# Optimization experiments

Measured on AMD Instinct MI355X. Metric: run time of the kernel, lower is better.

Reference implementation:

```python
import jax, jax.numpy as jnp
import numpy as np

N_NODES = 50000
N_EDGES = 800000
IN_DIM = 128
HEADS = 4
OUT_DIM = 32
NEG_SLOPE = 0.2


def setup_inputs() -> dict:
    key = jax.random.key(0)
    k_x, k_e, k_w, k_as, k_ad = jax.random.split(key, 5)
    x = jax.random.normal(k_x, (N_NODES, IN_DIM), dtype=jnp.float32)
    edge_index = jax.random.randint(k_e, (2, N_EDGES), 0, N_NODES, dtype=jnp.int32)
    # Linear(in_dim, heads*out_dim, bias=False): store as [in_dim, heads*out_dim]
    W = jax.random.normal(k_w, (IN_DIM, HEADS * OUT_DIM), dtype=jnp.float32) * 0.05
    a_src = jax.random.normal(k_as, (HEADS, OUT_DIM), dtype=jnp.float32) * 0.01
    a_dst = jax.random.normal(k_ad, (HEADS, OUT_DIM), dtype=jnp.float32) * 0.01
    return {"x": x, "edge_index": edge_index, "W": W, "a_src": a_src, "a_dst": a_dst}


def reference(x, edge_index, W, a_src, a_dst):
    N = x.shape[0]
    H, D = a_src.shape
    src, dst = edge_index[0], edge_index[1]
    h = (x @ W).reshape(N, H, D)                      # [N, H, D]
    h_src = h[src]                                    # [E, H, D] gather
    h_dst = h[dst]                                    # [E, H, D] gather
    e = jnp.einsum('ehd,hd->eh', h_src, a_src) + jnp.einsum('ehd,hd->eh', h_dst, a_dst)
    e = jax.nn.leaky_relu(e, NEG_SLOPE)               # [E, H]
    # segment softmax over dst, per head (vectorized across heads)
    m = jax.ops.segment_max(e, dst, num_segments=N)   # [N, H]
    exp = jnp.exp(e - m[dst])                         # [E, H]
    s = jax.ops.segment_sum(exp, dst, num_segments=N) # [N, H]
    alpha = exp / (s[dst] + 1e-12)                    # [E, H]
    # dropout p=0.0 -> identity
    out = jax.ops.segment_sum(alpha[:, :, None] * h_src, dst, num_segments=N)  # [N, H, D]
    return out.mean(axis=1)                           # [N, D]
```

## Files before the change

### kernel.cpp

```cpp
#include <hip/hip_runtime.h>
#include <hip/hip_bf16.h>

#define IN_DIM 128
#define HEADS 4
#define ODIM 32
#define HD (HEADS * ODIM)
#define NEG_SLOPE 0.2f

#define GM 64
#define LDK 136
#define ACCW 132

#define BIN_SHIFT 5
#define BIN_NODES 32
#define BINCAP 1024
#define MAXBINS 2048
#define KE 16

#define SMEM_BYTES 52224

typedef unsigned short ushortT;
typedef __attribute__((ext_vector_type(8))) short bf16x8;
typedef __attribute__((ext_vector_type(4))) float f32x4;

static __device__ __forceinline__ ushortT f2bf(float f) {
    __hip_bfloat16 b = __float2bfloat16(f);
    return *reinterpret_cast<ushortT*>(&b);
}
static __device__ __forceinline__ float hsel(float4 v, int head) {
    return (head == 0) ? v.x : (head == 1) ? v.y : (head == 2) ? v.z : v.w;
}
static __device__ __forceinline__ float i8f(unsigned int p, int sh) {
    return (float)((int)(p << (24 - sh)) >> 24);
}

__global__ void __launch_bounds__(256) k_wconv_zero(
    const float* __restrict__ W, ushortT* __restrict__ Wt_g,
    int* __restrict__ bin_cursor, int nbins)
{
    const int idx = blockIdx.x * 256 + threadIdx.x;
    const int c = idx >> 7, k = idx & 127;
    Wt_g[c * 128 + k] = f2bf(W[k * HD + c]);
    if (idx < nbins) bin_cursor[idx] = 0;
}

__global__ void __launch_bounds__(256) k_mega(
    const float* __restrict__ x, const ushortT* __restrict__ Wt_g,
    const float* __restrict__ a_src, const float* __restrict__ a_dst,
    const int* __restrict__ src, const int* __restrict__ dst,
    unsigned char* __restrict__ h8, float* __restrict__ scales,
    float* __restrict__ s_src, float* __restrict__ s_dst,
    int* __restrict__ bin_cursor, int* __restrict__ bin_buf,
    int N, int E, int nbins, int nBinBlocks)
{
    __shared__ __align__(16) char smem[SMEM_BYTES];
    const int t = threadIdx.x;

    if ((int)blockIdx.x < nBinBlocks) {
        int* lcnt = reinterpret_cast<int*>(smem);
        int* lcur = lcnt + MAXBINS;
        for (int i = t; i < nbins; i += 256) lcnt[i] = 0;
        __syncthreads();

        const int base_e = blockIdx.x * (256 * KE);
        int b_[KE]; int p_[KE];
#pragma unroll
        for (int k = 0; k < KE; ++k) {
            const int e = base_e + k * 256 + t;
            if (e < E) {
                const int d = dst[e];
                const int s = src[e];
                b_[k] = d >> BIN_SHIFT;
                p_[k] = ((d & (BIN_NODES - 1)) << 16) | s;
                atomicAdd(&lcnt[b_[k]], 1);
            } else {
                b_[k] = -1;
            }
        }
        __syncthreads();
        for (int i = t; i < nbins; i += 256) {
            const int c = lcnt[i];
            lcur[i] = (c > 0) ? atomicAdd(&bin_cursor[i], c) : 0;
        }
        __syncthreads();
#pragma unroll
        for (int k = 0; k < KE; ++k) {
            if (b_[k] >= 0) {
                const int pos = atomicAdd(&lcur[b_[k]], 1);
                if (pos < BINCAP) bin_buf[b_[k] * BINCAP + pos] = p_[k];
            }
        }
        return;
    }

    ushortT* Xs = reinterpret_cast<ushortT*>(smem);
    ushortT* Wt = Xs + GM * LDK;

    const int n0 = ((int)blockIdx.x - nBinBlocks) * GM;

    {
#pragma unroll
        for (int it = 0; it < 8; ++it) {
            const int o = it * 2048 + t * 8;
            *reinterpret_cast<uint4*>(&Wt[(o >> 7) * LDK + (o & 127)]) =
                *reinterpret_cast<const uint4*>(&Wt_g[o]);
        }
    }
    {
        const int r  = t >> 2;
        const int k0 = (t & 3) * 32;
        const int ng = n0 + r;
        if (ng < N) {
#pragma unroll
            for (int kk = 0; kk < 32; kk += 4) {
                float4 v = *reinterpret_cast<const float4*>(
                    &x[(size_t)ng * IN_DIM + k0 + kk]);
                ushort4 u;
                u.x = f2bf(v.x); u.y = f2bf(v.y); u.z = f2bf(v.z); u.w = f2bf(v.w);
                *reinterpret_cast<ushort4*>(&Xs[r * LDK + k0 + kk]) = u;
            }
        } else {
#pragma unroll
            for (int kk = 0; kk < 32; kk += 4)
                *reinterpret_cast<ushort4*>(&Xs[r * LDK + k0 + kk]) =
                    make_ushort4(0, 0, 0, 0);
        }
    }
    __syncthreads();

    const int w  = t >> 6;
    const int l  = t & 63;
    const int lr = l & 15;
    const int lk = (l >> 4) * 8;

    f32x4 acc[8];
#pragma unroll
    for (int i = 0; i < 8; ++i) acc[i] = (f32x4)(0.f);

#pragma unroll
    for (int kt = 0; kt < 4; ++kt) {
        const bf16x8 af = *reinterpret_cast<const bf16x8*>(
            &Xs[(w * 16 + lr) * LDK + kt * 32 + lk]);
#pragma unroll
        for (int ct = 0; ct < 8; ++ct) {
            const bf16x8 bfr = *reinterpret_cast<const bf16x8*>(
                &Wt[(ct * 16 + lr) * LDK + kt * 32 + lk]);
            acc[ct] = __builtin_amdgcn_mfma_f32_16x16x32_bf16(af, bfr, acc[ct],
                                                              0, 0, 0);
        }
    }

    float aSv[8], aDv[8];
#pragma unroll
    for (int ct = 0; ct < 8; ++ct) {
        aSv[ct] = a_src[ct * 16 + lr];
        aDv[ct] = a_dst[ct * 16 + lr];
    }
    const int rbase = w * 16 + (l >> 4) * 4;

#pragma unroll
    for (int j = 0; j < 4; ++j) {
        const int ng = n0 + rbase + j;
        float ps[4] = {0.f, 0.f, 0.f, 0.f}, pd[4] = {0.f, 0.f, 0.f, 0.f};
#pragma unroll
        for (int ct = 0; ct < 8; ++ct) {
            ps[ct >> 1] = fmaf(acc[ct][j], aSv[ct], ps[ct >> 1]);
            pd[ct >> 1] = fmaf(acc[ct][j], aDv[ct], pd[ct >> 1]);
        }
#pragma unroll
        for (int o = 1; o <= 8; o <<= 1) {
#pragma unroll
            for (int hh = 0; hh < 4; ++hh) {
                ps[hh] += __shfl_xor(ps[hh], o, 64);
                pd[hh] += __shfl_xor(pd[hh], o, 64);
            }
        }
        if (lr == 0 && ng < N) {
            *reinterpret_cast<float4*>(&s_src[ng * 4]) =
                make_float4(ps[0], ps[1], ps[2], ps[3]);
            *reinterpret_cast<float4*>(&s_dst[ng * 4]) =
                make_float4(pd[0], pd[1], pd[2], pd[3]);
        }
    }

    __syncthreads();
    float* accb = reinterpret_cast<float*>(smem);

#pragma unroll
    for (int ct = 0; ct < 8; ++ct)
#pragma unroll
        for (int j = 0; j < 4; ++j)
            accb[(rbase + j) * ACCW + ct * 16 + lr] = acc[ct][j];
    __syncthreads();

    {
        const int row = t >> 2;
        const int c0  = (t & 3) * 32;
        const int ng  = n0 + row;

        float4 v[8];
        float m = 0.f;
#pragma unroll
        for (int i = 0; i < 8; ++i) {
            v[i] = *reinterpret_cast<const float4*>(&accb[row * ACCW + c0 + 4 * i]);
            m = fmaxf(m, fmaxf(fmaxf(fabsf(v[i].x), fabsf(v[i].y)),
                               fmaxf(fabsf(v[i].z), fabsf(v[i].w))));
        }
        m = fmaxf(m, __shfl_xor(m, 1, 64));
        m = fmaxf(m, __shfl_xor(m, 2, 64));

        const float inv = (m > 0.f) ? 127.f / m : 0.f;
        unsigned int p[8];
#pragma unroll
        for (int i = 0; i < 8; ++i) {
            const int q0 = __float2int_rn(v[i].x * inv);
            const int q1 = __float2int_rn(v[i].y * inv);
            const int q2 = __float2int_rn(v[i].z * inv);
            const int q3 = __float2int_rn(v[i].w * inv);
            p[i] = (q0 & 0xFF) | ((q1 & 0xFF) << 8) |
                   ((q2 & 0xFF) << 16) | ((q3 & 0xFF) << 24);
        }
        if (ng < N) {
            *reinterpret_cast<uint4*>(&h8[(size_t)ng * 128 + c0]) =
                make_uint4(p[0], p[1], p[2], p[3]);
            *reinterpret_cast<uint4*>(&h8[(size_t)ng * 128 + c0 + 16]) =
                make_uint4(p[4], p[5], p[6], p[7]);
            if ((t & 3) == 0) scales[ng] = m * (1.f / 127.f);
        }
    }
}

__global__ void __launch_bounds__(256) k_pull_binned(
    const int* __restrict__ bin_buf, const int* __restrict__ bin_cursor,
    const unsigned char* __restrict__ h8, const float* __restrict__ scales,
    const float* __restrict__ s_src, const float* __restrict__ s_dst,
    float* __restrict__ out, int N)
{
    __shared__ ushortT csr[BINCAP];
    __shared__ int cnt_s[BIN_NODES], start_s[BIN_NODES], cur_s[BIN_NODES];

    const int b = blockIdx.x;
    const int t = threadIdx.x;
    const int node0 = b << BIN_SHIFT;

    int nedge = bin_cursor[b];
    nedge = (nedge < BINCAP) ? nedge : BINCAP;

    if (t < BIN_NODES) cnt_s[t] = 0;
    __syncthreads();

    for (int i = t; i < nedge; i += 256)
        atomicAdd(&cnt_s[bin_buf[b * BINCAP + i] >> 16], 1);
    __syncthreads();

    if (t < 32) {
        const int v = cnt_s[t];
        int inc = v;
#pragma unroll
        for (int o = 1; o < 32; o <<= 1) {
            const int x = __shfl_up(inc, o, 32);
            if (t >= o) inc += x;
        }
        start_s[t] = inc - v;
        cur_s[t]   = inc - v;
    }
    __syncthreads();

    for (int i = t; i < nedge; i += 256) {
        const int p = bin_buf[b * BINCAP + i];
        const int pos = atomicAdd(&cur_s[p >> 16], 1);
        csr[pos] = (ushortT)(p & 0xFFFF);
    }
    __syncthreads();

    const int wv   = t >> 6;
    const int l    = t & 63;
    const int half = l >> 5;
    const int l32  = l & 31;
    const int head = l32 >> 3;
    const int hoff = head * 8 + (l32 & 7);

    const unsigned int* hu = reinterpret_cast<const unsigned int*>(h8);
    const float4* ss4 = reinterpret_cast<const float4*>(s_src);

    for (int k = 0; k < 8; ++k) {
        const int nloc = wv * 8 + k;
        const int n = node0 + nloc;
        if (n >= N) break;

        const int st  = start_s[nloc];
        const int deg = cnt_s[nloc];
        const float4 vd4 = reinterpret_cast<const float4*>(s_dst)[n];
        const float vd = hsel(vd4, head);

        float den = 0.f;
        float a0 = 0.f, a1 = 0.f, a2 = 0.f, a3 = 0.f;

        const int count = (deg - half + 1) >> 1;
        for (int j = 0; j < count; j += 4) {
            const int i0 = st + 2 * j + half;
            const bool v1 = (j + 1) < count;
            const bool v2 = (j + 2) < count;
            const bool v3 = (j + 3) < count;
            const int s0 = csr[i0];
            const int s1 = v1 ? csr[i0 + 2] : s0;
            const int s2 = v2 ? csr[i0 + 4] : s0;
            const int s3 = v3 ? csr[i0 + 6] : s0;

            const float4 w0 = ss4[s0];
            const float4 w1 = ss4[s1];
            const float4 w2 = ss4[s2];
            const float4 w3 = ss4[s3];
            const float sc0 = scales[s0];
            const float sc1 = scales[s1];
            const float sc2 = scales[s2];
            const float sc3 = scales[s3];
            const unsigned int q0 = hu[(size_t)s0 * 32 + hoff];
            const unsigned int q1 = hu[(size_t)s1 * 32 + hoff];
            const unsigned int q2 = hu[(size_t)s2 * 32 + hoff];
            const unsigned int q3 = hu[(size_t)s3 * 32 + hoff];

            float e0 = hsel(w0, head) + vd;
            float e1 = hsel(w1, head) + vd;
            float e2 = hsel(w2, head) + vd;
            float e3 = hsel(w3, head) + vd;
            e0 = (e0 > 0.f) ? e0 : NEG_SLOPE * e0;
            e1 = (e1 > 0.f) ? e1 : NEG_SLOPE * e1;
            e2 = (e2 > 0.f) ? e2 : NEG_SLOPE * e2;
            e3 = (e3 > 0.f) ? e3 : NEG_SLOPE * e3;
            const float x0 = __expf(e0);
            const float x1 = v1 ? __expf(e1) : 0.f;
            const float x2 = v2 ? __expf(e2) : 0.f;
            const float x3 = v3 ? __expf(e3) : 0.f;

            den += (x0 + x1) + (x2 + x3);
            const float ws0 = x0 * sc0;
            const float ws1 = x1 * sc1;
            const float ws2 = x2 * sc2;
            const float ws3 = x3 * sc3;

            a0 = fmaf(ws0, i8f(q0, 0), a0);  a1 = fmaf(ws0, i8f(q0, 8), a1);
            a2 = fmaf(ws0, i8f(q0, 16), a2); a3 = fmaf(ws0, i8f(q0, 24), a3);
            a0 = fmaf(ws1, i8f(q1, 0), a0);  a1 = fmaf(ws1, i8f(q1, 8), a1);
            a2 = fmaf(ws1, i8f(q1, 16), a2); a3 = fmaf(ws1, i8f(q1, 24), a3);
            a0 = fmaf(ws2, i8f(q2, 0), a0);  a1 = fmaf(ws2, i8f(q2, 8), a1);
            a2 = fmaf(ws2, i8f(q2, 16), a2); a3 = fmaf(ws2, i8f(q2, 24), a3);
            a0 = fmaf(ws3, i8f(q3, 0), a0);  a1 = fmaf(ws3, i8f(q3, 8), a1);
            a2 = fmaf(ws3, i8f(q3, 16), a2); a3 = fmaf(ws3, i8f(q3, 24), a3);
        }

        a0 += __shfl_xor(a0, 32, 64);
        a1 += __shfl_xor(a1, 32, 64);
        a2 += __shfl_xor(a2, 32, 64);
        a3 += __shfl_xor(a3, 32, 64);
        den += __shfl_xor(den, 32, 64);

        const float inv = 1.f / (den + 1e-12f);
        a0 *= inv; a1 *= inv; a2 *= inv; a3 *= inv;

        a0 += __shfl_xor(a0, 8, 64);  a0 += __shfl_xor(a0, 16, 64);
        a1 += __shfl_xor(a1, 8, 64);  a1 += __shfl_xor(a1, 16, 64);
        a2 += __shfl_xor(a2, 8, 64);  a2 += __shfl_xor(a2, 16, 64);
        a3 += __shfl_xor(a3, 8, 64);  a3 += __shfl_xor(a3, 16, 64);

        if (l < 8) {
            float4 o4 = make_float4(0.25f * a0, 0.25f * a1, 0.25f * a2, 0.25f * a3);
            *reinterpret_cast<float4*>(&out[(size_t)n * ODIM + l * 4]) = o4;
        }
    }
}

extern "C" void kernel_launch(void* const* d_in, const int* in_sizes, int n_in,
                              void* d_out, int out_size, void* d_ws, size_t ws_size,
                              hipStream_t stream)
{
    const float* x      = (const float*)d_in[0];
    const int*   eidx   = (const int*)d_in[1];
    const float* W      = (const float*)d_in[2];
    const float* a_src  = (const float*)d_in[3];
    const float* a_dst  = (const float*)d_in[4];
    float* out = (float*)d_out;

    const int N = in_sizes[0] / IN_DIM;
    const int E = in_sizes[1] / 2;
    const int* src = eidx;
    const int* dst = eidx + E;

    const int nbins = (N + BIN_NODES - 1) >> BIN_SHIFT;

    char* wsp = (char*)d_ws;
    unsigned char* h8 = (unsigned char*)wsp; wsp += (size_t)N * 128;
    float* scales   = (float*)wsp;    wsp += (size_t)N * sizeof(float);
    float* s_src    = (float*)wsp;    wsp += (size_t)N * HEADS * sizeof(float);
    float* s_dst    = (float*)wsp;    wsp += (size_t)N * HEADS * sizeof(float);
    ushortT* Wt_g   = (ushortT*)wsp;  wsp += (size_t)128 * 128 * sizeof(ushortT);
    int* bin_buf    = (int*)wsp;      wsp += (size_t)nbins * BINCAP * sizeof(int);
    int* bin_cursor = (int*)wsp;      wsp += (size_t)nbins * sizeof(int);

    k_wconv_zero<<<64, 256, 0, stream>>>(W, Wt_g, bin_cursor, nbins);

    {
        const int epb = 256 * KE;
        const int nBinBlocks  = (E + epb - 1) / epb;
        const int nGemmBlocks = (N + GM - 1) / GM;
        k_mega<<<nBinBlocks + nGemmBlocks, 256, 0, stream>>>(
            x, Wt_g, a_src, a_dst, src, dst,
            h8, scales, s_src, s_dst, bin_cursor, bin_buf,
            N, E, nbins, nBinBlocks);
    }

    k_pull_binned<<<nbins, 256, 0, stream>>>(bin_buf, bin_cursor, h8, scales,
                                             s_src, s_dst, out, N);
}
```

Measured before the change: 74.00 us.

## Stage per-edge exp weights and quantized source rows in shared memory

During the CSR scatter, each block now computes the per-edge attention exponentials for all four heads and the source scales once, storing them in LDS. A cooperative pass then copies each edge's 128-byte int8 source row into LDS with 16-byte loads. The per-node accumulation loop reads from LDS instead of issuing scattered global gathers, falling back to global loads beyond 512 edges. This aims to replace many small latency-bound gathers with coalesced row loads, at the cost of about 75KB of LDS per block, which lowers occupancy, plus an extra synchronisation.

Result: slower. 124.2 us (+67.9%).

```diff
diff --git a/kernel.cpp b/kernel.cpp
--- a/kernel.cpp
+++ b/kernel.cpp
@@ -14,6 +14,8 @@
 #define BIN_SHIFT 5
 #define BIN_NODES 32
 #define BINCAP 1024
+#define SCAP 512
+#define ROWW 33
 #define MAXBINS 2048
 #define KE 16
 
@@ -238,6 +240,9 @@
 {
     __shared__ ushortT csr[BINCAP];
     __shared__ int cnt_s[BIN_NODES], start_s[BIN_NODES], cur_s[BIN_NODES];
+    __shared__ unsigned int rows[SCAP * ROWW];
+    __shared__ float wexp[SCAP * HEADS];
+    __shared__ float wsc[SCAP];
 
     const int b = blockIdx.x;
     const int t = threadIdx.x;
@@ -246,6 +251,10 @@
     int nedge = bin_cursor[b];
     nedge = (nedge < BINCAP) ? nedge : BINCAP;
 
+    const float4* ss4 = reinterpret_cast<const float4*>(s_src);
+    const float4* sd4 = reinterpret_cast<const float4*>(s_dst);
+    const unsigned int* hu = reinterpret_cast<const unsigned int*>(h8);
+
     if (t < BIN_NODES) cnt_s[t] = 0;
     __syncthreads();
 
@@ -268,8 +277,37 @@
 
     for (int i = t; i < nedge; i += 256) {
         const int p = bin_buf[b * BINCAP + i];
-        const int pos = atomicAdd(&cur_s[p >> 16], 1);
-        csr[pos] = (ushortT)(p & 0xFFFF);
+        const int s = p & 0xFFFF;
+        const int dloc = p >> 16;
+        const int pos = atomicAdd(&cur_s[dloc], 1);
+        csr[pos] = (ushortT)s;
+        if (pos < SCAP) {
+            const float4 vs = ss4[s];
+            const float4 vd = sd4[node0 + dloc];
+            float e0 = vs.x + vd.x, e1 = vs.y + vd.y;
+            float e2 = vs.z + vd.z, e3 = vs.w + vd.w;
+            e0 = (e0 > 0.f) ? e0 : NEG_SLOPE * e0;
+            e1 = (e1 > 0.f) ? e1 : NEG_SLOPE * e1;
+            e2 = (e2 > 0.f) ? e2 : NEG_SLOPE * e2;
+            e3 = (e3 > 0.f) ? e3 : NEG_SLOPE * e3;
+            wexp[pos * 4 + 0] = __expf(e0);
+            wexp[pos * 4 + 1] = __expf(e1);
+            wexp[pos * 4 + 2] = __expf(e2);
+            wexp[pos * 4 + 3] = __expf(e3);
+            wsc[pos] = scales[s];
+        }
+    }
+    __syncthreads();
+
+    {
+        const int cap = (nedge < SCAP) ? nedge : SCAP;
+        const int sub = (t & 7) * 4;
+        for (int i = t >> 3; i < cap; i += 32) {
+            const int s = csr[i];
+            const uint4 v = *reinterpret_cast<const uint4*>(
+                &hu[(size_t)s * 32 + sub]);
+            *reinterpret_cast<uint4*>(&rows[i * ROWW + sub]) = v;
+        }
     }
     __syncthreads();
 
@@ -280,9 +318,6 @@
     const int head = l32 >> 3;
     const int hoff = head * 8 + (l32 & 7);
 
-    const unsigned int* hu = reinterpret_cast<const unsigned int*>(h8);
-    const float4* ss4 = reinterpret_cast<const float4*>(s_src);
-
     for (int k = 0; k < 8; ++k) {
         const int nloc = wv * 8 + k;
         const int n = node0 + nloc;
@@ -290,7 +325,7 @@
 
         const int st  = start_s[nloc];
         const int deg = cnt_s[nloc];
-        const float4 vd4 = reinterpret_cast<const float4*>(s_dst)[n];
+        const float4 vd4 = sd4[n];
         const float vd = hsel(vd4, head);
 
         float den = 0.f;
@@ -298,55 +333,31 @@
 
         const int count = (deg - half + 1) >> 1;
         for (int j = 0; j < count; j += 4) {
-            const int i0 = st + 2 * j + half;
-            const bool v1 = (j + 1) < count;
-            const bool v2 = (j + 2) < count;
-            const bool v3 = (j + 3) < count;
-            const int s0 = csr[i0];
-            const int s1 = v1 ? csr[i0 + 2] : s0;
-            const int s2 = v2 ? csr[i0 + 4] : s0;
-            const int s3 = v3 ? csr[i0 + 6] : s0;
-
-            const float4 w0 = ss4[s0];
-            const float4 w1 = ss4[s1];
-            const float4 w2 = ss4[s2];
-            const float4 w3 = ss4[s3];
-            const float sc0 = scales[s0];
-            const float sc1 = scales[s1];
-            const float sc2 = scales[s2];
-            const float sc3 = scales[s3];
-            const unsigned int q0 = hu[(size_t)s0 * 32 + hoff];
-            const unsigned int q1 = hu[(size_t)s1 * 32 + hoff];
-            const unsigned int q2 = hu[(size_t)s2 * 32 + hoff];
-            const unsigned int q3 = hu[(size_t)s3 * 32 + hoff];
-
-            float e0 = hsel(w0, head) + vd;
-            float e1 = hsel(w1, head) + vd;
-            float e2 = hsel(w2, head) + vd;
-            float e3 = hsel(w3, head) + vd;
-            e0 = (e0 > 0.f) ? e0 : NEG_SLOPE * e0;
-            e1 = (e1 > 0.f) ? e1 : NEG_SLOPE * e1;
-            e2 = (e2 > 0.f) ? e2 : NEG_SLOPE * e2;
-            e3 = (e3 > 0.f) ? e3 : NEG_SLOPE * e3;
-            const float x0 = __expf(e0);
-            const float x1 = v1 ? __expf(e1) : 0.f;
-            const float x2 = v2 ? __expf(e2) : 0.f;
-            const float x3 = v3 ? __expf(e3) : 0.f;
-
-            den += (x0 + x1) + (x2 + x3);
-            const float ws0 = x0 * sc0;
-            const float ws1 = x1 * sc1;
-            const float ws2 = x2 * sc2;
-            const float ws3 = x3 * sc3;
-
-            a0 = fmaf(ws0, i8f(q0, 0), a0);  a1 = fmaf(ws0, i8f(q0, 8), a1);
-            a2 = fmaf(ws0, i8f(q0, 16), a2); a3 = fmaf(ws0, i8f(q0, 24), a3);
-            a0 = fmaf(ws1, i8f(q1, 0), a0);  a1 = fmaf(ws1, i8f(q1, 8), a1);
-            a2 = fmaf(ws1, i8f(q1, 16), a2); a3 = fmaf(ws1, i8f(q1, 24), a3);
-            a0 = fmaf(ws2, i8f(q2, 0), a0);  a1 = fmaf(ws2, i8f(q2, 8), a1);
-            a2 = fmaf(ws2, i8f(q2, 16), a2); a3 = fmaf(ws2, i8f(q2, 24), a3);
-            a0 = fmaf(ws3, i8f(q3, 0), a0);  a1 = fmaf(ws3, i8f(q3, 8), a1);
-            a2 = fmaf(ws3, i8f(q3, 16), a2); a3 = fmaf(ws3, i8f(q3, 24), a3);
+#pragma unroll
+            for (int m = 0; m < 4; ++m) {
+                const bool vm = (j + m) < count;
+                const int i0 = st + 2 * (vm ? (j + m) : j) + half;
+                float ex, sc; unsigned int q;
+                if (i0 < SCAP) {
+                    ex = wexp[i0 * 4 + head];
+                    sc = wsc[i0];
+                    q  = rows[i0 * ROWW + hoff];
+                } else {
+                    const int s = csr[i0];
+                    float e = hsel(ss4[s], head) + vd;
+                    e = (e > 0.f) ? e : NEG_SLOPE * e;
+                    ex = __expf(e);
+                    sc = scales[s];
+                    q  = hu[(size_t)s * 32 + hoff];
+                }
+                ex = vm ? ex : 0.f;
+                den += ex;
+                const float ws = ex * sc;
+                a0 = fmaf(ws, i8f(q, 0), a0);
+                a1 = fmaf(ws, i8f(q, 8), a1);
+                a2 = fmaf(ws, i8f(q, 16), a2);
+                a3 = fmaf(ws, i8f(q, 24), a3);
+            }
         }
 
         a0 += __shfl_xor(a0, 32, 64);
```
